# Kernel optimization log

Measured on AMD Instinct MI355X. Metric: run time of the kernel, lower is better.

## Reference

```python
import jax, jax.numpy as jnp
import numpy as np
import math

BLOCK_SIZE = 128  # config.block_size


def setup_inputs() -> dict:
    key = jax.random.key(0)
    k1, k2, k3 = jax.random.split(key, 3)
    B, H, S, D = 2, 12, 4096, 64
    return {
        "query_layer": jax.random.normal(k1, (B, H, S, D), dtype=jnp.float32),
        "key_layer": jax.random.normal(k2, (B, H, S, D), dtype=jnp.float32),
        "value_layer": jax.random.normal(k3, (B, H, S, D), dtype=jnp.float32),
        "attention_mask": jnp.zeros((B, 1, 1, S), dtype=jnp.float32),
    }


def reference(query_layer, key_layer, value_layer, attention_mask):
    d = query_layer.shape[-1]
    # [B,H,S,S] attention scores
    scores = jnp.einsum("bhqd,bhkd->bhqk", query_layer, key_layer) / math.sqrt(d)
    scores = scores + attention_mask
    # Faithful to source: the bottom-right block is OVERWRITTEN with
    # tril(ones, -1).T * finfo.min  (0 on/below diag, min strictly above)
    bs = BLOCK_SIZE
    causal_mask = jnp.tril(jnp.ones((bs, bs), dtype=scores.dtype), k=-1).T
    causal_mask = causal_mask * jnp.finfo(scores.dtype).min
    scores = scores.at[..., -bs:, -bs:].set(causal_mask)
    probs = jax.nn.softmax(scores, axis=-1)
    # dropout is identity in eval mode
    return jnp.einsum("bhqk,bhkd->bhqd", probs, value_layer)
```

## Files before the change

kernel.cpp:

```cpp
#include <hip/hip_runtime.h>

#define S_LEN 4096
#define DH    64
#define BQ    128
#define BK    64
#define NTILE (S_LEN / BK)
#define QBLKS (S_LEN / BQ)
#define NBH   24
#define NHEADS 12

typedef __attribute__((ext_vector_type(8))) short short8;
typedef __attribute__((ext_vector_type(4))) short short4v;
typedef __attribute__((ext_vector_type(4))) float f32x4;

#define PSTR 72
#define KSTR 72
#define VSTR 72
#define LOG2E 1.44269504088896f
#define MCONST (-12.99718425f)

#define NKCH (NBH * S_LEN * DH / 8)
#define WS_NEEDED ((size_t)NKCH * 16 * 2 + 2 * (size_t)S_LEN * 4)

__device__ __forceinline__ short f2bf(float x) {
    unsigned u = __builtin_bit_cast(unsigned, x);
    return (short)((u + 0x8000u) >> 16);
}

__global__ __launch_bounds__(256)
void prepass(const float* __restrict__ K, const float* __restrict__ V,
             const float* __restrict__ M, short* __restrict__ Kf,
             short* __restrict__ Vtf, float* __restrict__ Mf)
{
    __shared__ __align__(16) short K_lds[BK * KSTR];
    __shared__ __align__(16) short Vt_lds[DH * VSTR];

    const int tid = threadIdx.x;
    const int bh  = blockIdx.x >> 6;
    const int t   = blockIdx.x & 63;
    const size_t base = ((size_t)bh * S_LEN + (size_t)t * BK) * DH;

    #pragma unroll
    for (int it = 0; it < 4; ++it) {
        int idx = tid + 256 * it;
        int row = idx >> 4, c4 = idx & 15;
        float4 v = *(const float4*)(K + base + (size_t)row * DH + 4 * c4);
        short4v b4 = { f2bf(v.x), f2bf(v.y), f2bf(v.z), f2bf(v.w) };
        *(short4v*)&K_lds[row * KSTR + 4 * c4] = b4;
    }
    {
        int kb = tid >> 4, db = tid & 15;
        const float* vp = V + base + (size_t)(4 * kb) * DH + 4 * db;
        float4 r0 = *(const float4*)(vp);
        float4 r1 = *(const float4*)(vp + DH);
        float4 r2 = *(const float4*)(vp + 2 * DH);
        float4 r3 = *(const float4*)(vp + 3 * DH);
        short4v c0 = { f2bf(r0.x), f2bf(r1.x), f2bf(r2.x), f2bf(r3.x) };
        short4v c1 = { f2bf(r0.y), f2bf(r1.y), f2bf(r2.y), f2bf(r3.y) };
        short4v c2 = { f2bf(r0.z), f2bf(r1.z), f2bf(r2.z), f2bf(r3.z) };
        short4v c3 = { f2bf(r0.w), f2bf(r1.w), f2bf(r2.w), f2bf(r3.w) };
        *(short4v*)&Vt_lds[(4 * db + 0) * VSTR + 4 * kb] = c0;
        *(short4v*)&Vt_lds[(4 * db + 1) * VSTR + 4 * kb] = c1;
        *(short4v*)&Vt_lds[(4 * db + 2) * VSTR + 4 * kb] = c2;
        *(short4v*)&Vt_lds[(4 * db + 3) * VSTR + 4 * kb] = c3;
    }
    __syncthreads();

    const size_t obase = (size_t)(bh * NTILE + t) * 4096;
    #pragma unroll
    for (int e = 0; e < 2; ++e) {
        int ci = tid + 256 * e;
        int lane = ci & 63, n = lane & 15, q = lane >> 4;
        {
            int kt = (ci >> 6) & 1, mt = ci >> 7;
            short8 f = *(const short8*)&K_lds[(16 * mt + n) * KSTR + 32 * kt + 8 * q];
            *(short8*)&Kf[obase + (size_t)ci * 8] = f;
        }
        {
            int d = (ci >> 6) & 3, kt2 = (ci >> 8) & 1;
            short8 g = *(const short8*)&Vt_lds[(16 * d + n) * VSTR + 32 * kt2 + 8 * q];
            *(short8*)&Vtf[obase + (size_t)ci * 8] = g;
        }
    }
    if ((bh % NHEADS) == 0 && tid < 16) {
        int b_idx = bh / NHEADS;
        float4 mv = *(const float4*)(M + (size_t)b_idx * S_LEN + t * BK + 4 * tid);
        mv.x = mv.x * LOG2E + MCONST;
        mv.y = mv.y * LOG2E + MCONST;
        mv.z = mv.z * LOG2E + MCONST;
        mv.w = mv.w * LOG2E + MCONST;
        *(float4*)&Mf[(size_t)b_idx * S_LEN + t * BK + 4 * tid] = mv;
    }
}

__global__ __launch_bounds__(256, 3)
void fa3(const float* __restrict__ Q, const short* __restrict__ Kf,
         const short* __restrict__ Vtf, const float* __restrict__ Mf,
         float* __restrict__ O)
{
    __shared__ __align__(16) short P_lds[BQ * PSTR];

    const int tid  = threadIdx.x;
    const int w    = tid >> 6;
    const int lane = tid & 63;
    const int n    = lane & 15;
    const int quad = lane >> 4;

    const int bid  = blockIdx.x;
    const int x    = bid & 7;
    const int g    = bid >> 3;
    const int bh   = x + 8 * (g >> 5);
    const int qblk = g & 31;
    const bool special = (qblk == QBLKS - 1);

    const size_t base  = (size_t)bh * S_LEN * DH;
    const int    b_idx = bh / NHEADS;

    const float QSCALE = 0.125f * LOG2E;
    const int q0 = qblk * BQ + w * 32;
    short8 qf[2][2];
    #pragma unroll
    for (int s = 0; s < 2; ++s) {
        const float* qp = Q + base + (size_t)(q0 + 16 * s + n) * DH;
        #pragma unroll
        for (int kt = 0; kt < 2; ++kt) {
            const float* p = qp + 32 * kt + 8 * quad;
            float4 a = *(const float4*)p;
            float4 b = *(const float4*)(p + 4);
            short8 f;
            f[0] = f2bf(a.x * QSCALE); f[1] = f2bf(a.y * QSCALE);
            f[2] = f2bf(a.z * QSCALE); f[3] = f2bf(a.w * QSCALE);
            f[4] = f2bf(b.x * QSCALE); f[5] = f2bf(b.y * QSCALE);
            f[6] = f2bf(b.z * QSCALE); f[7] = f2bf(b.w * QSCALE);
            qf[s][kt] = f;
        }
    }

    f32x4 o[4][2];
    #pragma unroll
    for (int d = 0; d < 4; ++d)
        #pragma unroll
        for (int s = 0; s < 2; ++s) o[d][s] = (f32x4){0.f, 0.f, 0.f, 0.f};
    f32x4 lsum[2] = { (f32x4){0.f,0.f,0.f,0.f}, (f32x4){0.f,0.f,0.f,0.f} };

    const short8 ONES = { 0x3F80, 0x3F80, 0x3F80, 0x3F80,
                          0x3F80, 0x3F80, 0x3F80, 0x3F80 };
    const float* mrow = Mf + (size_t)b_idx * S_LEN;

    for (int t = 0; t < NTILE; ++t) {
        if (special && t >= NTILE - 2) {
            #pragma unroll
            for (int s = 0; s < 2; ++s) {
                int ql = w * 32 + 16 * s + n;
                int qrow = ql;
                #pragma unroll
                for (int mt = 0; mt < 4; ++mt) {
                    int k0 = (t - (NTILE - 2)) * BK + 16 * mt + 4 * quad;
                    unsigned d0 = (k0     > ql ? 0u : 0x3900u)
                                | (k0 + 1 > ql ? 0u : 0x39000000u);
                    unsigned d1 = (k0 + 2 > ql ? 0u : 0x3900u)
                                | (k0 + 3 > ql ? 0u : 0x39000000u);
                    *(uint2*)&P_lds[qrow * PSTR + 16 * mt + 4 * quad] = make_uint2(d0, d1);
                }
            }
        } else {
            const short* kb = Kf + (size_t)(bh * NTILE + t) * 4096 + (size_t)lane * 8;
            short8 kfr[4][2];
            #pragma unroll
            for (int mt = 0; mt < 4; ++mt)
                #pragma unroll
                for (int kt = 0; kt < 2; ++kt)
                    kfr[mt][kt] = *(const short8*)(kb + (mt * 2 + kt) * 512);
            f32x4 mk[4];
            #pragma unroll
            for (int mt = 0; mt < 4; ++mt)
                mk[mt] = *(const f32x4*)(mrow + t * BK + 16 * mt + 4 * quad);

            f32x4 acc[4][2];
            #pragma unroll
            for (int mt = 0; mt < 4; ++mt)
                #pragma unroll
                for (int s = 0; s < 2; ++s) {
                    f32x4 c = (f32x4){0.f, 0.f, 0.f, 0.f};
                    c = __builtin_amdgcn_mfma_f32_16x16x32_bf16(kfr[mt][0], qf[s][0], c, 0, 0, 0);
                    c = __builtin_amdgcn_mfma_f32_16x16x32_bf16(kfr[mt][1], qf[s][1], c, 0, 0, 0);
                    acc[mt][s] = c;
                }

            #pragma unroll
            for (int s = 0; s < 2; ++s) {
                int qrow = w * 32 + 16 * s + n;
                #pragma unroll
                for (int mt = 0; mt < 4; ++mt) {
                    float p0 = __builtin_amdgcn_exp2f(acc[mt][s][0] + mk[mt][0]);
                    float p1 = __builtin_amdgcn_exp2f(acc[mt][s][1] + mk[mt][1]);
                    float p2 = __builtin_amdgcn_exp2f(acc[mt][s][2] + mk[mt][2]);
                    float p3 = __builtin_amdgcn_exp2f(acc[mt][s][3] + mk[mt][3]);
                    unsigned d0 = __builtin_amdgcn_perm(
                        __builtin_bit_cast(unsigned, p1),
                        __builtin_bit_cast(unsigned, p0), 0x07060302u);
                    unsigned d1 = __builtin_amdgcn_perm(
                        __builtin_bit_cast(unsigned, p3),
                        __builtin_bit_cast(unsigned, p2), 0x07060302u);
                    *(uint2*)&P_lds[qrow * PSTR + 16 * mt + 4 * quad] = make_uint2(d0, d1);
                }
            }
        }

        const short* vb = Vtf + (size_t)(bh * NTILE + t) * 4096 + (size_t)lane * 8;
        short8 vfr[2][4];
        #pragma unroll
        for (int kt2 = 0; kt2 < 2; ++kt2)
            #pragma unroll
            for (int d = 0; d < 4; ++d)
                vfr[kt2][d] = *(const short8*)(vb + (kt2 * 4 + d) * 512);

        #pragma unroll
        for (int kt2 = 0; kt2 < 2; ++kt2) {
            short8 pf0 = *(const short8*)&P_lds[(w * 32 + n) * PSTR + 32 * kt2 + 8 * quad];
            short8 pf1 = *(const short8*)&P_lds[(w * 32 + 16 + n) * PSTR + 32 * kt2 + 8 * quad];
            lsum[0] = __builtin_amdgcn_mfma_f32_16x16x32_bf16(ONES, pf0, lsum[0], 0, 0, 0);
            lsum[1] = __builtin_amdgcn_mfma_f32_16x16x32_bf16(ONES, pf1, lsum[1], 0, 0, 0);
            #pragma unroll
            for (int d = 0; d < 4; ++d) {
                o[d][0] = __builtin_amdgcn_mfma_f32_16x16x32_bf16(vfr[kt2][d], pf0, o[d][0], 0, 0, 0);
                o[d][1] = __builtin_amdgcn_mfma_f32_16x16x32_bf16(vfr[kt2][d], pf1, o[d][1], 0, 0, 0);
            }
        }
    }

    #pragma unroll
    for (int s = 0; s < 2; ++s) {
        float inv = 1.0f / lsum[s][0];
        int qg = q0 + 16 * s + n;
        float* op = O + base + (size_t)qg * DH;
        #pragma unroll
        for (int d = 0; d < 4; ++d) {
            f32x4 r = o[d][s] * inv;
            *(f32x4*)(op + 16 * d + 4 * quad) = r;
        }
    }
}

extern "C" void kernel_launch(void* const* d_in, const int* in_sizes, int n_in,
                              void* d_out, int out_size, void* d_ws, size_t ws_size,
                              hipStream_t stream) {
    const float* Q = (const float*)d_in[0];
    const float* K = (const float*)d_in[1];
    const float* V = (const float*)d_in[2];
    const float* M = (const float*)d_in[3];
    float* O = (float*)d_out;

    short* Kf  = (short*)d_ws;
    short* Vtf = Kf + (size_t)NKCH * 8;
    float* Mf  = (float*)(Vtf + (size_t)NKCH * 8);

    prepass<<<dim3(NBH * NTILE), dim3(256), 0, stream>>>(K, V, M, Kf, Vtf, Mf);
    fa3<<<dim3(NBH * QBLKS), dim3(256), 0, stream>>>(Q, Kf, Vtf, Mf, O);
}
```

Before: 255.2 us.

## Interleave K/V fragments per lane and software-prefetch next K tile

```diff
diff --git a/kernel.cpp b/kernel.cpp
--- a/kernel.cpp
+++ b/kernel.cpp
@@ -19,8 +19,8 @@
 #define LOG2E 1.44269504088896f
 #define MCONST (-12.99718425f)
 
-#define NKCH (NBH * S_LEN * DH / 8)
-#define WS_NEEDED ((size_t)NKCH * 16 * 2 + 2 * (size_t)S_LEN * 4)
+#define TILE_SHORTS 8192
+#define KV_SHORTS ((size_t)NBH * NTILE * TILE_SHORTS)
 
 __device__ __forceinline__ short f2bf(float x) {
     unsigned u = __builtin_bit_cast(unsigned, x);
@@ -29,8 +29,8 @@
 
 __global__ __launch_bounds__(256)
 void prepass(const float* __restrict__ K, const float* __restrict__ V,
-             const float* __restrict__ M, short* __restrict__ Kf,
-             short* __restrict__ Vtf, float* __restrict__ Mf)
+             const float* __restrict__ M, short* __restrict__ KV,
+             float* __restrict__ Mf)
 {
     __shared__ __align__(16) short K_lds[BK * KSTR];
     __shared__ __align__(16) short Vt_lds[DH * VSTR];
@@ -66,22 +66,23 @@
     }
     __syncthreads();
 
-    const size_t obase = (size_t)(bh * NTILE + t) * 4096;
-    #pragma unroll
-    for (int e = 0; e < 2; ++e) {
-        int ci = tid + 256 * e;
-        int lane = ci & 63, n = lane & 15, q = lane >> 4;
-        {
-            int kt = (ci >> 6) & 1, mt = ci >> 7;
-            short8 f = *(const short8*)&K_lds[(16 * mt + n) * KSTR + 32 * kt + 8 * q];
-            *(short8*)&Kf[obase + (size_t)ci * 8] = f;
-        }
-        {
-            int d = (ci >> 6) & 3, kt2 = (ci >> 8) & 1;
-            short8 g = *(const short8*)&Vt_lds[(16 * d + n) * VSTR + 32 * kt2 + 8 * q];
-            *(short8*)&Vtf[obase + (size_t)ci * 8] = g;
-        }
-    }
+    const size_t tile_s = (size_t)(bh * NTILE + t) * TILE_SHORTS;
+    const int lane = tid & 63, n = lane & 15, q = lane >> 4;
+    const int cbase = 4 * (tid >> 6);
+    #pragma unroll
+    for (int i = 0; i < 4; ++i) {
+        int c = cbase + i;
+        short8 val;
+        if (c < 8) {
+            int mt = c >> 1, kt = c & 1;
+            val = *(const short8*)&K_lds[(16 * mt + n) * KSTR + 32 * kt + 8 * q];
+        } else {
+            int cv = c - 8, kt2 = cv >> 2, d = cv & 3;
+            val = *(const short8*)&Vt_lds[(16 * d + n) * VSTR + 32 * kt2 + 8 * q];
+        }
+        *(short8*)&KV[tile_s + (size_t)lane * 128 + c * 8] = val;
+    }
+
     if ((bh % NHEADS) == 0 && tid < 16) {
         int b_idx = bh / NHEADS;
         float4 mv = *(const float4*)(M + (size_t)b_idx * S_LEN + t * BK + 4 * tid);
@@ -94,9 +95,8 @@
 }
 
 __global__ __launch_bounds__(256, 3)
-void fa3(const float* __restrict__ Q, const short* __restrict__ Kf,
-         const short* __restrict__ Vtf, const float* __restrict__ Mf,
-         float* __restrict__ O)
+void fa4(const float* __restrict__ Q, const short* __restrict__ KV,
+         const float* __restrict__ Mf, float* __restrict__ O)
 {
     __shared__ __align__(16) short P_lds[BQ * PSTR];
 
@@ -146,56 +146,63 @@
     const short8 ONES = { 0x3F80, 0x3F80, 0x3F80, 0x3F80,
                           0x3F80, 0x3F80, 0x3F80, 0x3F80 };
     const float* mrow = Mf + (size_t)b_idx * S_LEN;
+    const short* KVb  = KV + (size_t)(bh * NTILE) * TILE_SHORTS;
+    const int loff = lane * 128;
+
+    short8 kfr[8];
+    f32x4  mkr[4];
+    {
+        const short8* pl = (const short8*)(KVb + loff);
+        #pragma unroll
+        for (int i = 0; i < 8; ++i) kfr[i] = pl[i];
+        #pragma unroll
+        for (int mt = 0; mt < 4; ++mt)
+            mkr[mt] = *(const f32x4*)(mrow + 16 * mt + 4 * quad);
+    }
 
     for (int t = 0; t < NTILE; ++t) {
-        if (special && t >= NTILE - 2) {
-            #pragma unroll
-            for (int s = 0; s < 2; ++s) {
-                int ql = w * 32 + 16 * s + n;
-                int qrow = ql;
-                #pragma unroll
-                for (int mt = 0; mt < 4; ++mt) {
-                    int k0 = (t - (NTILE - 2)) * BK + 16 * mt + 4 * quad;
-                    unsigned d0 = (k0     > ql ? 0u : 0x3900u)
-                                | (k0 + 1 > ql ? 0u : 0x39000000u);
-                    unsigned d1 = (k0 + 2 > ql ? 0u : 0x3900u)
-                                | (k0 + 3 > ql ? 0u : 0x39000000u);
-                    *(uint2*)&P_lds[qrow * PSTR + 16 * mt + 4 * quad] = make_uint2(d0, d1);
-                }
-            }
-        } else {
-            const short* kb = Kf + (size_t)(bh * NTILE + t) * 4096 + (size_t)lane * 8;
-            short8 kfr[4][2];
-            #pragma unroll
-            for (int mt = 0; mt < 4; ++mt)
-                #pragma unroll
-                for (int kt = 0; kt < 2; ++kt)
-                    kfr[mt][kt] = *(const short8*)(kb + (mt * 2 + kt) * 512);
-            f32x4 mk[4];
-            #pragma unroll
-            for (int mt = 0; mt < 4; ++mt)
-                mk[mt] = *(const f32x4*)(mrow + t * BK + 16 * mt + 4 * quad);
-
-            f32x4 acc[4][2];
+        const bool sp = special && t >= NTILE - 2;
+
+        short8 vfr[8];
+        {
+            const short8* pl = (const short8*)(KVb + (size_t)t * TILE_SHORTS + loff);
+            #pragma unroll
+            for (int i = 0; i < 8; ++i) vfr[i] = pl[8 + i];
+        }
+
+        f32x4 acc[4][2];
+        if (!sp) {
             #pragma unroll
             for (int mt = 0; mt < 4; ++mt)
                 #pragma unroll
                 for (int s = 0; s < 2; ++s) {
-                    f32x4 c = (f32x4){0.f, 0.f, 0.f, 0.f};
-                    c = __builtin_amdgcn_mfma_f32_16x16x32_bf16(kfr[mt][0], qf[s][0], c, 0, 0, 0);
-                    c = __builtin_amdgcn_mfma_f32_16x16x32_bf16(kfr[mt][1], qf[s][1], c, 0, 0, 0);
+                    f32x4 c = mkr[mt];
+                    c = __builtin_amdgcn_mfma_f32_16x16x32_bf16(kfr[2 * mt],     qf[s][0], c, 0, 0, 0);
+                    c = __builtin_amdgcn_mfma_f32_16x16x32_bf16(kfr[2 * mt + 1], qf[s][1], c, 0, 0, 0);
                     acc[mt][s] = c;
                 }
-
+        }
+
+        {
+            int tn = (t + 1 < NTILE) ? t + 1 : t;
+            const short8* ql = (const short8*)(KVb + (size_t)tn * TILE_SHORTS + loff);
+            #pragma unroll
+            for (int i = 0; i < 8; ++i) kfr[i] = ql[i];
+            #pragma unroll
+            for (int mt = 0; mt < 4; ++mt)
+                mkr[mt] = *(const f32x4*)(mrow + tn * BK + 16 * mt + 4 * quad);
+        }
+
+        if (!sp) {
             #pragma unroll
             for (int s = 0; s < 2; ++s) {
                 int qrow = w * 32 + 16 * s + n;
                 #pragma unroll
                 for (int mt = 0; mt < 4; ++mt) {
-                    float p0 = __builtin_amdgcn_exp2f(acc[mt][s][0] + mk[mt][0]);
-                    float p1 = __builtin_amdgcn_exp2f(acc[mt][s][1] + mk[mt][1]);
-                    float p2 = __builtin_amdgcn_exp2f(acc[mt][s][2] + mk[mt][2]);
-                    float p3 = __builtin_amdgcn_exp2f(acc[mt][s][3] + mk[mt][3]);
+                    float p0 = __builtin_amdgcn_exp2f(acc[mt][s][0]);
+                    float p1 = __builtin_amdgcn_exp2f(acc[mt][s][1]);
+                    float p2 = __builtin_amdgcn_exp2f(acc[mt][s][2]);
+                    float p3 = __builtin_amdgcn_exp2f(acc[mt][s][3]);
                     unsigned d0 = __builtin_amdgcn_perm(
                         __builtin_bit_cast(unsigned, p1),
                         __builtin_bit_cast(unsigned, p0), 0x07060302u);
@@ -205,15 +212,21 @@
                     *(uint2*)&P_lds[qrow * PSTR + 16 * mt + 4 * quad] = make_uint2(d0, d1);
                 }
             }
-        }
-
-        const short* vb = Vtf + (size_t)(bh * NTILE + t) * 4096 + (size_t)lane * 8;
-        short8 vfr[2][4];
-        #pragma unroll
-        for (int kt2 = 0; kt2 < 2; ++kt2)
-            #pragma unroll
-            for (int d = 0; d < 4; ++d)
-                vfr[kt2][d] = *(const short8*)(vb + (kt2 * 4 + d) * 512);
+        } else {
+            #pragma unroll
+            for (int s = 0; s < 2; ++s) {
+                int ql2 = w * 32 + 16 * s + n;
+                #pragma unroll
+                for (int mt = 0; mt < 4; ++mt) {
+                    int k0 = (t - (NTILE - 2)) * BK + 16 * mt + 4 * quad;
+                    unsigned d0 = (k0     > ql2 ? 0u : 0x3900u)
+                                | (k0 + 1 > ql2 ? 0u : 0x39000000u);
+                    unsigned d1 = (k0 + 2 > ql2 ? 0u : 0x3900u)
+                                | (k0 + 3 > ql2 ? 0u : 0x39000000u);
+                    *(uint2*)&P_lds[ql2 * PSTR + 16 * mt + 4 * quad] = make_uint2(d0, d1);
+                }
+            }
+        }
 
         #pragma unroll
         for (int kt2 = 0; kt2 < 2; ++kt2) {
@@ -223,8 +236,8 @@
             lsum[1] = __builtin_amdgcn_mfma_f32_16x16x32_bf16(ONES, pf1, lsum[1], 0, 0, 0);
             #pragma unroll
             for (int d = 0; d < 4; ++d) {
-                o[d][0] = __builtin_amdgcn_mfma_f32_16x16x32_bf16(vfr[kt2][d], pf0, o[d][0], 0, 0, 0);
-                o[d][1] = __builtin_amdgcn_mfma_f32_16x16x32_bf16(vfr[kt2][d], pf1, o[d][1], 0, 0, 0);
+                o[d][0] = __builtin_amdgcn_mfma_f32_16x16x32_bf16(vfr[kt2 * 4 + d], pf0, o[d][0], 0, 0, 0);
+                o[d][1] = __builtin_amdgcn_mfma_f32_16x16x32_bf16(vfr[kt2 * 4 + d], pf1, o[d][1], 0, 0, 0);
             }
         }
     }
@@ -251,10 +264,9 @@
     const float* M = (const float*)d_in[3];
     float* O = (float*)d_out;
 
-    short* Kf  = (short*)d_ws;
-    short* Vtf = Kf + (size_t)NKCH * 8;
-    float* Mf  = (float*)(Vtf + (size_t)NKCH * 8);
-
-    prepass<<<dim3(NBH * NTILE), dim3(256), 0, stream>>>(K, V, M, Kf, Vtf, Mf);
-    fa3<<<dim3(NBH * QBLKS), dim3(256), 0, stream>>>(Q, Kf, Vtf, Mf, O);
-}
+    short* KV = (short*)d_ws;
+    float* Mf = (float*)(KV + KV_SHORTS);
+
+    prepass<<<dim3(NBH * NTILE), dim3(256), 0, stream>>>(K, V, M, KV, Mf);
+    fa4<<<dim3(NBH * QBLKS), dim3(256), 0, stream>>>(Q, KV, Mf, O);
+}
```

Result: slower. 480.6 us (+88.3%).

## Stage K/V tiles in double-buffered LDS via async global-to-LDS loads

Applied to the files above, without the earlier changes.

```diff
diff --git a/kernel.cpp b/kernel.cpp
--- a/kernel.cpp
+++ b/kernel.cpp
@@ -20,11 +20,16 @@
 #define MCONST (-12.99718425f)
 
 #define NKCH (NBH * S_LEN * DH / 8)
-#define WS_NEEDED ((size_t)NKCH * 16 * 2 + 2 * (size_t)S_LEN * 4)
 
 __device__ __forceinline__ short f2bf(float x) {
     unsigned u = __builtin_bit_cast(unsigned, x);
     return (short)((u + 0x8000u) >> 16);
+}
+
+typedef __attribute__((address_space(1))) const unsigned int guint;
+typedef __attribute__((address_space(3))) unsigned int luint;
+__device__ __forceinline__ void g2l16(const short* g, short* l) {
+    __builtin_amdgcn_global_load_lds((guint*)g, (luint*)l, 16, 0, 0);
 }
 
 __global__ __launch_bounds__(256)
@@ -78,8 +83,8 @@
         }
         {
             int d = (ci >> 6) & 3, kt2 = (ci >> 8) & 1;
-            short8 g = *(const short8*)&Vt_lds[(16 * d + n) * VSTR + 32 * kt2 + 8 * q];
-            *(short8*)&Vtf[obase + (size_t)ci * 8] = g;
+            short8 g2 = *(const short8*)&Vt_lds[(16 * d + n) * VSTR + 32 * kt2 + 8 * q];
+            *(short8*)&Vtf[obase + (size_t)ci * 8] = g2;
         }
     }
     if ((bh % NHEADS) == 0 && tid < 16) {
@@ -94,10 +99,12 @@
 }
 
 __global__ __launch_bounds__(256, 3)
-void fa3(const float* __restrict__ Q, const short* __restrict__ Kf,
+void fa6(const float* __restrict__ Q, const short* __restrict__ Kf,
          const short* __restrict__ Vtf, const float* __restrict__ Mf,
          float* __restrict__ O)
 {
+    __shared__ __align__(16) short Ks[2][4096];
+    __shared__ __align__(16) short Vs[2][4096];
     __shared__ __align__(16) short P_lds[BQ * PSTR];
 
     const int tid  = threadIdx.x;
@@ -146,56 +153,57 @@
     const short8 ONES = { 0x3F80, 0x3F80, 0x3F80, 0x3F80,
                           0x3F80, 0x3F80, 0x3F80, 0x3F80 };
     const float* mrow = Mf + (size_t)b_idx * S_LEN;
+    const short* Kg = Kf  + (size_t)(bh * NTILE) * 4096;
+    const short* Vg = Vtf + (size_t)(bh * NTILE) * 4096;
+
+    #pragma unroll
+    for (int i = 0; i < 2; ++i) {
+        int c = 2 * w + i;
+        g2l16(Kg + c * 512 + lane * 8, &Ks[0][c * 512]);
+        g2l16(Vg + c * 512 + lane * 8, &Vs[0][c * 512]);
+    }
+    __syncthreads();
 
     for (int t = 0; t < NTILE; ++t) {
-        if (special && t >= NTILE - 2) {
-            #pragma unroll
-            for (int s = 0; s < 2; ++s) {
-                int ql = w * 32 + 16 * s + n;
-                int qrow = ql;
-                #pragma unroll
-                for (int mt = 0; mt < 4; ++mt) {
-                    int k0 = (t - (NTILE - 2)) * BK + 16 * mt + 4 * quad;
-                    unsigned d0 = (k0     > ql ? 0u : 0x3900u)
-                                | (k0 + 1 > ql ? 0u : 0x39000000u);
-                    unsigned d1 = (k0 + 2 > ql ? 0u : 0x3900u)
-                                | (k0 + 3 > ql ? 0u : 0x39000000u);
-                    *(uint2*)&P_lds[qrow * PSTR + 16 * mt + 4 * quad] = make_uint2(d0, d1);
-                }
-            }
-        } else {
-            const short* kb = Kf + (size_t)(bh * NTILE + t) * 4096 + (size_t)lane * 8;
-            short8 kfr[4][2];
-            #pragma unroll
-            for (int mt = 0; mt < 4; ++mt)
-                #pragma unroll
-                for (int kt = 0; kt < 2; ++kt)
-                    kfr[mt][kt] = *(const short8*)(kb + (mt * 2 + kt) * 512);
-            f32x4 mk[4];
-            #pragma unroll
-            for (int mt = 0; mt < 4; ++mt)
-                mk[mt] = *(const f32x4*)(mrow + t * BK + 16 * mt + 4 * quad);
-
+        const bool sp = special && t >= NTILE - 2;
+        const int  cur = t & 1, nxt = cur ^ 1;
+
+        {
+            int tn = (t + 1 < NTILE) ? t + 1 : t;
+            const short* kg = Kg + (size_t)tn * 4096;
+            const short* vg = Vg + (size_t)tn * 4096;
+            #pragma unroll
+            for (int i = 0; i < 2; ++i) {
+                int c = 2 * w + i;
+                g2l16(kg + c * 512 + lane * 8, &Ks[nxt][c * 512]);
+                g2l16(vg + c * 512 + lane * 8, &Vs[nxt][c * 512]);
+            }
+        }
+
+        if (!sp) {
             f32x4 acc[4][2];
             #pragma unroll
-            for (int mt = 0; mt < 4; ++mt)
+            for (int mt = 0; mt < 4; ++mt) {
+                short8 k0 = *(const short8*)&Ks[cur][(2 * mt    ) * 512 + lane * 8];
+                short8 k1 = *(const short8*)&Ks[cur][(2 * mt + 1) * 512 + lane * 8];
+                f32x4 mk = *(const f32x4*)(mrow + t * BK + 16 * mt + 4 * quad);
                 #pragma unroll
                 for (int s = 0; s < 2; ++s) {
-                    f32x4 c = (f32x4){0.f, 0.f, 0.f, 0.f};
-                    c = __builtin_amdgcn_mfma_f32_16x16x32_bf16(kfr[mt][0], qf[s][0], c, 0, 0, 0);
-                    c = __builtin_amdgcn_mfma_f32_16x16x32_bf16(kfr[mt][1], qf[s][1], c, 0, 0, 0);
+                    f32x4 c = mk;
+                    c = __builtin_amdgcn_mfma_f32_16x16x32_bf16(k0, qf[s][0], c, 0, 0, 0);
+                    c = __builtin_amdgcn_mfma_f32_16x16x32_bf16(k1, qf[s][1], c, 0, 0, 0);
                     acc[mt][s] = c;
                 }
-
+            }
             #pragma unroll
             for (int s = 0; s < 2; ++s) {
                 int qrow = w * 32 + 16 * s + n;
                 #pragma unroll
                 for (int mt = 0; mt < 4; ++mt) {
-                    float p0 = __builtin_amdgcn_exp2f(acc[mt][s][0] + mk[mt][0]);
-                    float p1 = __builtin_amdgcn_exp2f(acc[mt][s][1] + mk[mt][1]);
-                    float p2 = __builtin_amdgcn_exp2f(acc[mt][s][2] + mk[mt][2]);
-                    float p3 = __builtin_amdgcn_exp2f(acc[mt][s][3] + mk[mt][3]);
+                    float p0 = __builtin_amdgcn_exp2f(acc[mt][s][0]);
+                    float p1 = __builtin_amdgcn_exp2f(acc[mt][s][1]);
+                    float p2 = __builtin_amdgcn_exp2f(acc[mt][s][2]);
+                    float p3 = __builtin_amdgcn_exp2f(acc[mt][s][3]);
                     unsigned d0 = __builtin_amdgcn_perm(
                         __builtin_bit_cast(unsigned, p1),
                         __builtin_bit_cast(unsigned, p0), 0x07060302u);
@@ -205,15 +213,21 @@
                     *(uint2*)&P_lds[qrow * PSTR + 16 * mt + 4 * quad] = make_uint2(d0, d1);
                 }
             }
-        }
-
-        const short* vb = Vtf + (size_t)(bh * NTILE + t) * 4096 + (size_t)lane * 8;
-        short8 vfr[2][4];
-        #pragma unroll
-        for (int kt2 = 0; kt2 < 2; ++kt2)
-            #pragma unroll
-            for (int d = 0; d < 4; ++d)
-                vfr[kt2][d] = *(const short8*)(vb + (kt2 * 4 + d) * 512);
+        } else {
+            #pragma unroll
+            for (int s = 0; s < 2; ++s) {
+                int ql2 = w * 32 + 16 * s + n;
+                #pragma unroll
+                for (int mt = 0; mt < 4; ++mt) {
+                    int k0 = (t - (NTILE - 2)) * BK + 16 * mt + 4 * quad;
+                    unsigned d0 = (k0     > ql2 ? 0u : 0x3900u)
+                                | (k0 + 1 > ql2 ? 0u : 0x39000000u);
+                    unsigned d1 = (k0 + 2 > ql2 ? 0u : 0x3900u)
+                                | (k0 + 3 > ql2 ? 0u : 0x39000000u);
+                    *(uint2*)&P_lds[ql2 * PSTR + 16 * mt + 4 * quad] = make_uint2(d0, d1);
+                }
+            }
+        }
 
         #pragma unroll
         for (int kt2 = 0; kt2 < 2; ++kt2) {
@@ -223,10 +237,13 @@
             lsum[1] = __builtin_amdgcn_mfma_f32_16x16x32_bf16(ONES, pf1, lsum[1], 0, 0, 0);
             #pragma unroll
             for (int d = 0; d < 4; ++d) {
-                o[d][0] = __builtin_amdgcn_mfma_f32_16x16x32_bf16(vfr[kt2][d], pf0, o[d][0], 0, 0, 0);
-                o[d][1] = __builtin_amdgcn_mfma_f32_16x16x32_bf16(vfr[kt2][d], pf1, o[d][1], 0, 0, 0);
-            }
-        }
+                short8 vf = *(const short8*)&Vs[cur][(kt2 * 4 + d) * 512 + lane * 8];
+                o[d][0] = __builtin_amdgcn_mfma_f32_16x16x32_bf16(vf, pf0, o[d][0], 0, 0, 0);
+                o[d][1] = __builtin_amdgcn_mfma_f32_16x16x32_bf16(vf, pf1, o[d][1], 0, 0, 0);
+            }
+        }
+
+        __syncthreads();
     }
 
     #pragma unroll
@@ -256,5 +273,5 @@
     float* Mf  = (float*)(Vtf + (size_t)NKCH * 8);
 
     prepass<<<dim3(NBH * NTILE), dim3(256), 0, stream>>>(K, V, M, Kf, Vtf, Mf);
-    fa3<<<dim3(NBH * QBLKS), dim3(256), 0, stream>>>(Q, Kf, Vtf, Mf, O);
-}
+    fa6<<<dim3(NBH * QBLKS), dim3(256), 0, stream>>>(Q, Kf, Vtf, Mf, O);
+}
```

New measurement: 228.8 us. 10.4% less time.
